# Kernel optimization log

Measured on AMD Instinct MI355X. Metric: run time of the kernel, lower is better.

Reference implementation:

```python
import jax, jax.numpy as jnp
import numpy as np

NUM_GROUPS = 8
EPS = 1e-5


def group_norm(x, gamma, beta):
    # x: [B, C, H, W]
    B, C, H, W = x.shape
    xg = x.reshape(B, NUM_GROUPS, C // NUM_GROUPS, H, W)
    mean = xg.mean(axis=(2, 3, 4), keepdims=True)
    var = xg.var(axis=(2, 3, 4), keepdims=True)
    xn = (xg - mean) * jax.lax.rsqrt(var + EPS)
    xn = xn.reshape(B, C, H, W)
    return xn * gamma[None, :, None, None] + beta[None, :, None, None]


def setup_inputs() -> dict:
    key = jax.random.key(0)
    ks = jax.random.split(key, 7)
    B, C, H, W = 4, 512, 64, 64
    x = jax.random.normal(ks[0], (B, C, H, W), dtype=jnp.float32)
    gamma = jnp.ones((C,), dtype=jnp.float32)
    beta = jnp.zeros((C,), dtype=jnp.float32)
    w_qkv = jax.random.normal(ks[1], (3 * C, C), dtype=jnp.float32) * (1.0 / np.sqrt(C))
    b_qkv = jax.random.normal(ks[2], (3 * C,), dtype=jnp.float32) * 0.01
    w_proj = jax.random.normal(ks[3], (C, C), dtype=jnp.float32) * (1.0 / np.sqrt(C))
    b_proj = jax.random.normal(ks[4], (C,), dtype=jnp.float32) * 0.01
    return {"x": x, "gamma": gamma, "beta": beta, "w_qkv": w_qkv,
            "b_qkv": b_qkv, "w_proj": w_proj, "b_proj": b_proj}


def reference(x, gamma, beta, w_qkv, b_qkv, w_proj, b_proj):
    B, C, H, W = x.shape
    N = H * W
    h = group_norm(x, gamma, beta)                       # [B,C,H,W]
    hf = h.reshape(B, C, N)                              # [B,C,N]
    # 1x1 conv == channel-wise linear map
    qkv = jnp.einsum('oc,bcn->bon', w_qkv, hf) + b_qkv[None, :, None]  # [B,3C,N]
    q, k, v = jnp.split(qkv, 3, axis=1)                  # each [B,C,N]
    q = q.transpose(0, 2, 1)                             # [B,N,C]
    v = v.transpose(0, 2, 1)                             # [B,N,C]
    scale = C ** (-0.5)
    attn = jax.nn.softmax(jnp.einsum('bnc,bcm->bnm', q, k) * scale, axis=-1)  # [B,N,N]
    out = jnp.einsum('bnm,bmc->bnc', attn, v)            # [B,N,C]
    out = out.transpose(0, 2, 1).reshape(B, C, H, W)
    proj = jnp.einsum('oc,bchw->bohw', w_proj, out) + b_proj[None, :, None, None]
    return x + proj
```

## Files before the change

kernel.cpp:

```cpp
#include <hip/hip_runtime.h>

typedef __attribute__((ext_vector_type(8))) short bf16x8;
typedef __attribute__((ext_vector_type(4))) float f32x4;
typedef __attribute__((ext_vector_type(4))) short s16x4;
using u16 = unsigned short;
using u8 = unsigned char;

#define DEVINL static __device__ __forceinline__

DEVINL u16 f2bf(float f) {
  union { float f; unsigned u; } v; v.f = f;
  unsigned r = v.u + 0x7FFFu + ((v.u >> 16) & 1u);
  return (u16)(r >> 16);
}

DEVINL u8 f2e4m3_sw(float f) {
  union { float f; unsigned u; } v; v.f = f;
  unsigned s = (v.u >> 24) & 0x80u;
  float a = fabsf(f);
  a = fminf(a, 448.f);
  union { float f; unsigned u; } b; b.f = a;
  unsigned bu = b.u + 0x7FFFFu + ((b.u >> 20) & 1u);
  unsigned e = bu >> 23;
  unsigned r;
  if (e >= 121) {
    r = ((e - 120) << 3) | ((bu >> 20) & 7u);
    if (r > 0x7Eu) r = 0x7Eu;
  } else {
    r = (unsigned)(a * 512.f + 0.5f);
    if (r > 7u) r = 8u;
  }
  return (u8)(r | s);
}

#if __has_builtin(__builtin_amdgcn_cvt_pk_fp8_f32)
DEVINL u8 f2e4m3(float f) {
  int p = __builtin_amdgcn_cvt_pk_fp8_f32(f, f, 0, false);
  return (u8)(p & 0xFF);
}
#else
DEVINL u8 f2e4m3(float f) { return f2e4m3_sw(f); }
#endif

DEVINL float bf2f(u16 h) {
  union { unsigned u; float f; } v; v.u = ((unsigned)h) << 16; return v.f;
}

DEVINL void gload16(const u16* g, u16* l) {
  __builtin_amdgcn_global_load_lds((const __attribute__((address_space(1))) void*)g,
                                   (__attribute__((address_space(3))) void*)l,
                                   16, 0, 0);
}
DEVINL void gload16b(const u8* g, u8* l) {
  __builtin_amdgcn_global_load_lds((const __attribute__((address_space(1))) void*)g,
                                   (__attribute__((address_space(3))) void*)l,
                                   16, 0, 0);
}

__global__ __launch_bounds__(256) void gn_stats1_k(const float* __restrict__ x,
                                                   float* __restrict__ psum,
                                                   float* __restrict__ psumsq) {
  const int blk = blockIdx.x;
  const float4* p4 = (const float4*)(x + (size_t)(blk >> 4) * (64 * 4096))
                     + (size_t)(blk & 15) * 4096;
  float s = 0.f, ss = 0.f;
  #pragma unroll
  for (int i = 0; i < 16; ++i) {
    float4 v = p4[i*256 + threadIdx.x];
    s  += v.x + v.y + v.z + v.w;
    ss += v.x*v.x + v.y*v.y + v.z*v.z + v.w*v.w;
  }
  #pragma unroll
  for (int off = 32; off > 0; off >>= 1) {
    s  += __shfl_down(s, off, 64);
    ss += __shfl_down(ss, off, 64);
  }
  __shared__ float rs[4], rss[4];
  const int lane = threadIdx.x & 63, w = threadIdx.x >> 6;
  if (lane == 0) { rs[w] = s; rss[w] = ss; }
  __syncthreads();
  if (threadIdx.x == 0) {
    psum[blk]   = rs[0]+rs[1]+rs[2]+rs[3];
    psumsq[blk] = rss[0]+rss[1]+rss[2]+rss[3];
  }
}

__global__ void gn_stats2_k(const float* __restrict__ psum,
                            const float* __restrict__ psumsq,
                            float* __restrict__ stats) {
  const int bg = threadIdx.x;
  if (bg >= 32) return;
  float s = 0.f, ss = 0.f;
  #pragma unroll
  for (int p = 0; p < 16; ++p) { s += psum[bg*16+p]; ss += psumsq[bg*16+p]; }
  const float inv = 1.f / 262144.f;
  float mean = s * inv;
  float var  = ss * inv - mean * mean;
  stats[bg*2]   = mean;
  stats[bg*2+1] = rsqrtf(var + 1e-5f);
}

__global__ __launch_bounds__(256) void gn_apply_k(const float* __restrict__ x,
                                                  const float* __restrict__ gamma,
                                                  const float* __restrict__ beta,
                                                  const float* __restrict__ stats,
                                                  u16* __restrict__ hT,
                                                  u8* __restrict__ hT8, int useF8) {
  __shared__ u16 tile[64][68];
  const int b = blockIdx.z, ct = blockIdx.y, nt = blockIdx.x;
  const int t = threadIdx.x;
  const float mean = stats[(b*8 + ct)*2 + 0];
  const float rstd = stats[(b*8 + ct)*2 + 1];
  const float* xb = x + ((size_t)b*512 + (size_t)ct*64) * 4096 + nt*64;
  #pragma unroll
  for (int i = 0; i < 4; ++i) {
    int idx = i*256 + t;
    int cl = idx >> 4, nl4 = idx & 15;
    float4 v = *(const float4*)(xb + (size_t)cl*4096 + nl4*4);
    float g = gamma[ct*64 + cl], bb = beta[ct*64 + cl];
    s16x4 o;
    o.x = (short)f2bf((v.x - mean) * rstd * g + bb);
    o.y = (short)f2bf((v.y - mean) * rstd * g + bb);
    o.z = (short)f2bf((v.z - mean) * rstd * g + bb);
    o.w = (short)f2bf((v.w - mean) * rstd * g + bb);
    *(s16x4*)(&tile[cl][nl4*4]) = o;
  }
  __syncthreads();
  if (useF8) {
    u8* o = hT8 + ((size_t)b*4096 + (size_t)nt*64) * 512 + ct*64;
    #pragma unroll
    for (int i = 0; i < 16; ++i) {
      int idx = i*256 + t; int nl = idx >> 6, cl = idx & 63;
      o[(size_t)nl*512 + cl] = f2e4m3(bf2f(tile[cl][nl]));
    }
  } else {
    u16* o = hT + ((size_t)b*4096 + (size_t)nt*64) * 512 + ct*64;
    #pragma unroll
    for (int i = 0; i < 16; ++i) {
      int idx = i*256 + t; int nl = idx >> 6, cl = idx & 63;
      o[(size_t)nl*512 + cl] = tile[cl][nl];
    }
  }
}

__global__ __launch_bounds__(256) void cast_w_k(const float* __restrict__ wq,
                                                const float* __restrict__ wp,
                                                u16* __restrict__ wqb,
                                                u16* __restrict__ wpb,
                                                u8* __restrict__ wq8,
                                                u8* __restrict__ wp8, int useF8) {
  int i = blockIdx.x*256 + threadIdx.x;
  if (useF8) {
    if (i < 1536*512) wq8[i] = f2e4m3(wq[i]);
    if (i < 512*512)  wp8[i] = f2e4m3(wp[i]);
  } else {
    if (i < 1536*512) wqb[i] = f2bf(wq[i]);
    if (i < 512*512)  wpb[i] = f2bf(wp[i]);
  }
}

DEVINL void gemm_nt_core(const u16* __restrict__ A, int lda,
                         const u16* __restrict__ B, int ldb,
                         int K, u16* As, u16* Bs, f32x4 acc[4][4]) {
  const int tid = threadIdx.x;
  const int lane = tid & 63, w = tid >> 6;
  const int wr = w >> 1, wc = w & 1;
  const int fr = lane & 15, fk = lane >> 4;
  for (int kt = 0; kt < K; kt += 64) {
    #pragma unroll
    for (int i = 0; i < 4; ++i) {
      int ch = i*256 + tid;
      int row = ch >> 3, kc = ch & 7;
      gload16(A + (size_t)row*lda + kt + kc*8, As + ch*8);
      gload16(B + (size_t)row*ldb + kt + kc*8, Bs + ch*8);
    }
    __syncthreads();
    #pragma unroll
    for (int kk = 0; kk < 2; ++kk) {
      bf16x8 af[4], bfg[4];
      #pragma unroll
      for (int i = 0; i < 4; ++i)
        af[i] = *(const bf16x8*)(As + ((wr*64 + i*16 + fr)*64 + kk*32 + fk*8));
      #pragma unroll
      for (int j = 0; j < 4; ++j)
        bfg[j] = *(const bf16x8*)(Bs + ((wc*64 + j*16 + fr)*64 + kk*32 + fk*8));
      #pragma unroll
      for (int i = 0; i < 4; ++i)
        #pragma unroll
        for (int j = 0; j < 4; ++j)
          acc[i][j] = __builtin_amdgcn_mfma_f32_16x16x32_bf16(af[i], bfg[j], acc[i][j], 0, 0, 0);
    }
    __syncthreads();
  }
}

#define GEMM_PROLOGUE() \
  __shared__ __align__(16) u16 As[128*64]; \
  __shared__ __align__(16) u16 Bs[128*64]; \
  f32x4 acc[4][4] = {}; \
  const int tid = threadIdx.x; \
  const int lane = tid & 63, w = tid >> 6; \
  const int wr = w >> 1, wc = w & 1; \
  const int fr = lane & 15, fk = lane >> 4; \
  (void)lane;

#define MFMA8(a, b, c) __builtin_amdgcn_mfma_f32_16x16x32_fp8_fp8((a), (b), (c), 0, 0, 0)

DEVINL void gemm_nt_f8(const u8* __restrict__ A, int lda,
                       const u8* __restrict__ B, int ldb,
                       int K, u8* Af, u8* Bf, f32x4 acc[4][4]) {
  const int tid = threadIdx.x;
  const int lane = tid & 63, w = tid >> 6;
  const int wr = w >> 1, wc = w & 1;
  const int fr = lane & 15, fk = lane >> 4;
  for (int kt = 0; kt < K; kt += 128) {
    #pragma unroll
    for (int q = 0; q < 4; ++q) {
      int c = q*256 + tid;
      int row = c >> 3, s16 = c & 7;
      int kc = s16 ^ ((row >> 1) & 7);
      gload16b(A + (size_t)row*lda + kt + kc*16, Af + c*16);
      gload16b(B + (size_t)row*ldb + kt + kc*16, Bf + c*16);
    }
    __syncthreads();
    #pragma unroll
    for (int kk = 0; kk < 4; ++kk) {
      long long a8[4], b8[4];
      #pragma unroll
      for (int i = 0; i < 4; ++i) {
        int row = wr*64 + i*16 + fr;
        int s16r = (kk*2 + (fk>>1)) ^ ((row>>1)&7);
        a8[i] = *(const long long*)(Af + row*128 + (s16r<<4) + ((fk&1)<<3));
      }
      #pragma unroll
      for (int j = 0; j < 4; ++j) {
        int row = wc*64 + j*16 + fr;
        int s16r = (kk*2 + (fk>>1)) ^ ((row>>1)&7);
        b8[j] = *(const long long*)(Bf + row*128 + (s16r<<4) + ((fk&1)<<3));
      }
      #pragma unroll
      for (int i = 0; i < 4; ++i)
        #pragma unroll
        for (int j = 0; j < 4; ++j)
          acc[i][j] = MFMA8(a8[i], b8[j], acc[i][j]);
    }
    __syncthreads();
  }
}

__global__ __launch_bounds__(256) void k_qkv(const u16* __restrict__ hT,
                                             const u16* __restrict__ wq,
                                             const float* __restrict__ bqkv,
                                             u16* __restrict__ qT, u16* __restrict__ kT,
                                             u16* __restrict__ vb) {
  GEMM_PROLOGUE();
  const int bz = blockIdx.z;
  const int rowBase = blockIdx.y * 128, colBase = blockIdx.x * 128;
  gemm_nt_core(hT + ((size_t)bz*4096 + rowBase)*512, 512,
               wq + (size_t)colBase*512, 512, 512, As, Bs, acc);
  #pragma unroll
  for (int i = 0; i < 4; ++i)
    #pragma unroll
    for (int j = 0; j < 4; ++j)
      #pragma unroll
      for (int r = 0; r < 4; ++r) {
        int n = rowBase + wr*64 + i*16 + fk*4 + r;
        int o = colBase + wc*64 + j*16 + fr;
        u16 u = f2bf(acc[i][j][r] + bqkv[o]);
        if (o < 512)       qT[((size_t)bz*4096 + n)*512 + o]          = u;
        else if (o < 1024) kT[((size_t)bz*4096 + n)*512 + (o - 512)]  = u;
        else               vb[((size_t)bz*512 + (o - 1024))*4096 + n] = u;
      }
}

__global__ __launch_bounds__(256) void k_qkv_f8(const u8* __restrict__ hT8,
                                                const u8* __restrict__ wq8,
                                                const float* __restrict__ bqkv,
                                                u8* __restrict__ qF8, u8* __restrict__ kF8,
                                                u8* __restrict__ vF8) {
  __shared__ __align__(16) u8 Af[128*128];
  __shared__ __align__(16) u8 Bf[128*128];
  f32x4 acc[4][4] = {};
  const int tid = threadIdx.x;
  const int lane = tid & 63, w = tid >> 6;
  const int wr = w >> 1, wc = w & 1;
  const int fr = lane & 15, fk = lane >> 4;
  const int bz = blockIdx.z;
  const int rowBase = blockIdx.y * 128, colBase = blockIdx.x * 128;
  gemm_nt_f8(hT8 + ((size_t)bz*4096 + rowBase)*512, 512,
             wq8 + (size_t)colBase*512, 512, 512, Af, Bf, acc);
  #pragma unroll
  for (int i = 0; i < 4; ++i)
    #pragma unroll
    for (int j = 0; j < 4; ++j)
      #pragma unroll
      for (int r = 0; r < 4; ++r) {
        int n = rowBase + wr*64 + i*16 + fk*4 + r;
        int o = colBase + wc*64 + j*16 + fr;
        u8 u = f2e4m3(acc[i][j][r] + bqkv[o]);
        if (o < 512)       qF8[((size_t)bz*4096 + n)*512 + o]          = u;
        else if (o < 1024) kF8[((size_t)bz*4096 + n)*512 + (o - 512)]  = u;
        else               vF8[((size_t)bz*512 + (o - 1024))*4096 + n] = u;
      }
}

__global__ __launch_bounds__(512) void k_scores_f8(const u8* __restrict__ qF8,
                                                   const u8* __restrict__ kF8,
                                                   u8* __restrict__ E8) {
  __shared__ __align__(16) u8 Af[128*64];
  __shared__ __align__(16) u8 Bf[128*64];
  f32x4 acc[2][4] = {};
  const int tid = threadIdx.x;
  const int lane = tid & 63, w = tid >> 6;
  const int wr = w >> 1, wc = w & 1;
  const int fr = lane & 15, fk = lane >> 4;
  const int bz = blockIdx.z;
  int f = blockIdx.y * 32 + blockIdx.x;
  int L = (f & 7) * 128 + (f >> 3);
  const int rowBase = (L >> 5) * 128, colBase = (L & 31) * 128;
  const u8* qa = qF8 + (size_t)bz*4096*512 + (size_t)rowBase*512;
  const u8* ka = kF8 + (size_t)bz*4096*512 + (size_t)colBase*512;
  u8* Eb = E8 + (size_t)bz*4096*4096;

  for (int kt = 0; kt < 512; kt += 64) {
    {
      int c = tid;
      int row = c >> 2, s16 = c & 3;
      int kc = s16 ^ ((row >> 1) & 3);
      gload16b(qa + (size_t)row*512 + kt + kc*16, Af + c*16);
      gload16b(ka + (size_t)row*512 + kt + kc*16, Bf + c*16);
    }
    __syncthreads();
    #pragma unroll
    for (int kk = 0; kk < 2; ++kk) {
      long long a8[2], b8[4];
      #pragma unroll
      for (int i = 0; i < 2; ++i) {
        int row = wr*32 + i*16 + fr;
        a8[i] = *(const long long*)(Af + row*64 +
                ((((kk*2 + (fk>>1)) ^ ((row>>1)&3)) << 4) | ((fk&1) << 3)));
      }
      #pragma unroll
      for (int j = 0; j < 4; ++j) {
        int row = wc*64 + j*16 + fr;
        b8[j] = *(const long long*)(Bf + row*64 +
                ((((kk*2 + (fk>>1)) ^ ((row>>1)&3)) << 4) | ((fk&1) << 3)));
      }
      #pragma unroll
      for (int i = 0; i < 2; ++i)
        #pragma unroll
        for (int j = 0; j < 4; ++j)
          acc[i][j] = MFMA8(a8[i], b8[j], acc[i][j]);
    }
    __syncthreads();
  }

  const float scale = 0.04419417382415922f;
  #pragma unroll
  for (int i = 0; i < 2; ++i)
    #pragma unroll
    for (int r = 0; r < 4; ++r) {
      int nl = rowBase + wr*32 + i*16 + fk*4 + r;
      #pragma unroll
      for (int j = 0; j < 4; ++j) {
        int m = colBase + wc*64 + j*16 + fr;
        Eb[(size_t)nl*4096 + m] = f2e4m3(__expf(acc[i][j][r] * scale));
      }
    }
}

__global__ __launch_bounds__(512) void k_pv_f8(const u8* __restrict__ E8,
                                               const u8* __restrict__ vF8,
                                               u8* __restrict__ attn8) {
  __shared__ __align__(16) u8 Af[128*128];
  __shared__ __align__(16) u8 Bf[128*128];
  f32x4 acc[2][4] = {};
  f32x4 acs[2] = {};
  const long long ONES = 0x3838383838383838LL;
  const int tid = threadIdx.x;
  const int lane = tid & 63, w = tid >> 6;
  const int wr = w >> 1, wc = w & 1;
  const int fr = lane & 15, fk = lane >> 4;
  const int bz = blockIdx.z;
  int f = blockIdx.y * 4 + blockIdx.x;
  int L = (f & 7) * 16 + (f >> 3);
  const int rowBase = (L >> 2) * 128, colBase = (L & 3) * 128;
  const u8* Eb = E8 + (size_t)bz*4096*4096 + (size_t)rowBase*4096;
  const u8* vbb = vF8 + (size_t)bz*512*4096 + (size_t)colBase*4096;
  u8* ab = attn8 + (size_t)bz*4096*512;

  for (int kt = 0; kt < 4096; kt += 128) {
    #pragma unroll
    for (int q = 0; q < 2; ++q) {
      int c = q*512 + tid;
      int row = c >> 3, s16 = c & 7;
      int kc = s16 ^ ((row >> 1) & 7);
      gload16b(Eb + (size_t)row*4096 + kt + kc*16, Af + c*16);
      gload16b(vbb + (size_t)row*4096 + kt + kc*16, Bf + c*16);
    }
    __syncthreads();
    #pragma unroll
    for (int kk = 0; kk < 4; ++kk) {
      long long a8[2], b8[4];
      #pragma unroll
      for (int i = 0; i < 2; ++i) {
        int row = wr*32 + i*16 + fr;
        int s16r = (kk*2 + (fk>>1)) ^ ((row>>1)&7);
        a8[i] = *(const long long*)(Af + row*128 + (s16r<<4) + ((fk&1)<<3));
      }
      #pragma unroll
      for (int j = 0; j < 4; ++j) {
        int row = wc*64 + j*16 + fr;
        int s16r = (kk*2 + (fk>>1)) ^ ((row>>1)&7);
        b8[j] = *(const long long*)(Bf + row*128 + (s16r<<4) + ((fk&1)<<3));
      }
      #pragma unroll
      for (int i = 0; i < 2; ++i) {
        #pragma unroll
        for (int j = 0; j < 4; ++j)
          acc[i][j] = MFMA8(a8[i], b8[j], acc[i][j]);
        acs[i] = MFMA8(a8[i], ONES, acs[i]);
      }
    }
    __syncthreads();
  }

  #pragma unroll
  for (int i = 0; i < 2; ++i)
    #pragma unroll
    for (int r = 0; r < 4; ++r) {
      int nl = rowBase + wr*32 + i*16 + fk*4 + r;
      float rinv = 1.0f / acs[i][r];
      #pragma unroll
      for (int j = 0; j < 4; ++j) {
        int d = colBase + wc*64 + j*16 + fr;
        ab[(size_t)nl*512 + d] = f2e4m3(acc[i][j][r] * rinv);
      }
    }
}

__global__ __launch_bounds__(256) void k_proj_f8(const u8* __restrict__ wp8,
                                                 const u8* __restrict__ attn8,
                                                 const float* __restrict__ bproj,
                                                 const float* __restrict__ x,
                                                 float* __restrict__ out) {
  __shared__ __align__(16) u8 Af[128*128];
  __shared__ __align__(16) u8 Bf[128*128];
  f32x4 acc[4][4] = {};
  const int tid = threadIdx.x;
  const int lane = tid & 63, w = tid >> 6;
  const int wr = w >> 1, wc = w & 1;
  const int fr = lane & 15, fk = lane >> 4;
  const int bz = blockIdx.z;
  const int rowBase = blockIdx.y * 128, colBase = blockIdx.x * 128;
  gemm_nt_f8(wp8 + (size_t)rowBase*512, 512,
             attn8 + ((size_t)bz*4096 + colBase)*512, 512, 512, Af, Bf, acc);
  #pragma unroll
  for (int i = 0; i < 4; ++i)
    #pragma unroll
    for (int j = 0; j < 4; ++j)
      #pragma unroll
      for (int r = 0; r < 4; ++r) {
        int o = rowBase + wr*64 + i*16 + fk*4 + r;
        int n = colBase + wc*64 + j*16 + fr;
        size_t idx = ((size_t)bz*512 + o)*4096 + n;
        out[idx] = acc[i][j][r] + bproj[o] + x[idx];
      }
}

__global__ __launch_bounds__(256) void k_scores(const u16* __restrict__ qT,
                                                const u16* __restrict__ kT,
                                                u16* __restrict__ E,
                                                float* __restrict__ lsum,
                                                long long qkStride, long long eStride,
                                                int lsStride) {
  GEMM_PROLOGUE();
  const int bz = blockIdx.z;
  const u16* q0 = qT + (size_t)bz * qkStride;
  const u16* k0 = kT + (size_t)bz * qkStride;
  u16* Eb = E + (size_t)bz * eStride;
  float* ls = lsum + (size_t)bz * lsStride;
  const int rowBase = blockIdx.y * 128, colBase = blockIdx.x * 128;
  gemm_nt_core(q0 + (size_t)rowBase*512, 512, k0 + (size_t)colBase*512, 512,
               512, As, Bs, acc);
  const float scale = 0.04419417382415922f;
  #pragma unroll
  for (int i = 0; i < 4; ++i)
    #pragma unroll
    for (int r = 0; r < 4; ++r) {
      int nl = rowBase + wr*64 + i*16 + fk*4 + r;
      float s = 0.f;
      #pragma unroll
      for (int j = 0; j < 4; ++j) {
        int m = colBase + wc*64 + j*16 + fr;
        float e = __expf(acc[i][j][r] * scale);
        Eb[(size_t)nl*4096 + m] = f2bf(e);
        s += e;
      }
      s += __shfl_xor(s, 1, 64);
      s += __shfl_xor(s, 2, 64);
      s += __shfl_xor(s, 4, 64);
      s += __shfl_xor(s, 8, 64);
      if (fr == 0) atomicAdd(&ls[nl], s);
    }
}

__global__ __launch_bounds__(256) void k_pv(const u16* __restrict__ E,
                                            const u16* __restrict__ vb,
                                            const float* __restrict__ lsum,
                                            u16* __restrict__ attnb,
                                            long long eStride, long long vStride,
                                            int lsStride, long long aStride) {
  GEMM_PROLOGUE();
  const int bz = blockIdx.z;
  const u16* Eb = E + (size_t)bz * eStride;
  const u16* vbb = vb + (size_t)bz * vStride;
  const float* ls = lsum + (size_t)bz * lsStride;
  u16* ab = attnb + (size_t)bz * aStride;
  const int rowBase = blockIdx.y * 128, colBase = blockIdx.x * 128;
  gemm_nt_core(Eb + (size_t)rowBase*4096, 4096, vbb + (size_t)colBase*4096, 4096,
               4096, As, Bs, acc);
  #pragma unroll
  for (int i = 0; i < 4; ++i)
    #pragma unroll
    for (int r = 0; r < 4; ++r) {
      int nl = rowBase + wr*64 + i*16 + fk*4 + r;
      float rinv = 1.0f / ls[nl];
      #pragma unroll
      for (int j = 0; j < 4; ++j) {
        int d = colBase + wc*64 + j*16 + fr;
        ab[(size_t)nl*512 + d] = f2bf(acc[i][j][r] * rinv);
      }
    }
}

__global__ __launch_bounds__(256) void k_proj(const u16* __restrict__ wp,
                                              const u16* __restrict__ attn,
                                              const float* __restrict__ bproj,
                                              const float* __restrict__ x,
                                              float* __restrict__ out) {
  GEMM_PROLOGUE();
  const int bz = blockIdx.z;
  const int rowBase = blockIdx.y * 128, colBase = blockIdx.x * 128;
  gemm_nt_core(wp + (size_t)rowBase*512, 512,
               attn + ((size_t)bz*4096 + colBase)*512, 512, 512, As, Bs, acc);
  #pragma unroll
  for (int i = 0; i < 4; ++i)
    #pragma unroll
    for (int j = 0; j < 4; ++j)
      #pragma unroll
      for (int r = 0; r < 4; ++r) {
        int o = rowBase + wr*64 + i*16 + fk*4 + r;
        int n = colBase + wc*64 + j*16 + fr;
        size_t idx = ((size_t)bz*512 + o)*4096 + n;
        out[idx] = acc[i][j][r] + bproj[o] + x[idx];
      }
}

extern "C" void kernel_launch(void* const* d_in, const int* in_sizes, int n_in,
                              void* d_out, int out_size, void* d_ws, size_t ws_size,
                              hipStream_t stream) {
  const float* x      = (const float*)d_in[0];
  const float* gamma  = (const float*)d_in[1];
  const float* beta   = (const float*)d_in[2];
  const float* w_qkv  = (const float*)d_in[3];
  const float* b_qkv  = (const float*)d_in[4];
  const float* w_proj = (const float*)d_in[5];
  const float* b_proj = (const float*)d_in[6];
  float* out = (float*)d_out;
  char* ws = (char*)d_ws;

  size_t off = 0;
  u16* wqb   = (u16*)(ws + off); off += (size_t)1536*512*2;
  u16* wpb   = (u16*)(ws + off); off += (size_t)512*512*2;
  u8*  wq8   = (u8*)(ws + off);  off += (size_t)1536*512;
  u8*  wp8   = (u8*)(ws + off);  off += (size_t)512*512;
  float* stats = (float*)(ws + off); off += 256;
  float* psum  = (float*)(ws + off); off += 512*4;
  float* psumsq= (float*)(ws + off); off += 512*4;
  float* lsum  = (float*)(ws + off); off += (size_t)4*4096*4;
  u16* hT    = (u16*)(ws + off);
  u16* attn  = hT;
  off += (size_t)4*4096*512*2;
  u16* qT    = (u16*)(ws + off); off += (size_t)4*4096*512*2;
  u16* kT    = (u16*)(ws + off); off += (size_t)4*4096*512*2;
  u16* vb    = (u16*)(ws + off); off += (size_t)4*4096*512*2;
  u16* E     = (u16*)(ws + off);
  size_t avail = ws_size > off ? ws_size - off : 0;
  const int useF8 = (avail >= (size_t)4*4096*4096) ? 1 : 0;
  u8* hT8  = (u8*)hT;
  u8* attn8 = hT8;
  u8* qF8 = (u8*)qT;
  u8* kF8 = (u8*)kT;
  u8* vF8 = (u8*)vb;
  u8* E8  = (u8*)E;

  gn_stats1_k<<<512, 256, 0, stream>>>(x, psum, psumsq);
  gn_stats2_k<<<1, 32, 0, stream>>>(psum, psumsq, stats);
  gn_apply_k<<<dim3(64, 8, 4), 256, 0, stream>>>(x, gamma, beta, stats, hT, hT8, useF8);
  cast_w_k<<<3072, 256, 0, stream>>>(w_qkv, w_proj, wqb, wpb, wq8, wp8, useF8);

  if (useF8) {
    k_qkv_f8<<<dim3(12, 32, 4), 256, 0, stream>>>(hT8, wq8, b_qkv, qF8, kF8, vF8);
    k_scores_f8<<<dim3(32, 32, 4), 512, 0, stream>>>(qF8, kF8, E8);
    k_pv_f8<<<dim3(4, 32, 4), 512, 0, stream>>>(E8, vF8, attn8);
    k_proj_f8<<<dim3(32, 4, 4), 256, 0, stream>>>(wp8, attn8, b_proj, x, out);
  } else {
    k_qkv<<<dim3(12, 32, 4), 256, 0, stream>>>(hT, wqb, b_qkv, qT, kT, vb);
    int CH = 4096;
    while (CH > 128 && (size_t)CH*4096*2 > avail) CH >>= 1;
    for (int b = 0; b < 4; ++b) {
      for (int c0 = 0; c0 < 4096; c0 += CH) {
        (void)hipMemsetAsync(lsum, 0, (size_t)CH * sizeof(float), stream);
        k_scores<<<dim3(32, CH/128, 1), 256, 0, stream>>>(
            qT + ((size_t)b*4096 + c0)*512, kT + (size_t)b*4096*512, E, lsum, 0, 0, 0);
        k_pv<<<dim3(4, CH/128, 1), 256, 0, stream>>>(
            E, vb + (size_t)b*512*4096, lsum, attn + ((size_t)b*4096 + c0)*512, 0, 0, 0, 0);
      }
    }
    k_proj<<<dim3(32, 4, 4), 256, 0, stream>>>(wpb, attn, b_proj, x, out);
  }
}
```

Baseline: 214.7 us.

## Double-buffer LDS tiles in FP8 scores and PV GEMM kernels

Both FP8 attention GEMM kernels now hold two LDS buffers for the A and B tiles. Each iteration prefetches the next K-slice into the alternate buffer while computing MFMAs on the current one. The goal is to hide global-to-LDS load latency behind compute and drop one barrier per iteration. In exchange, LDS footprint doubles (64KB per block in the PV kernel), which may limit occupancy.

```diff
diff --git a/kernel.cpp b/kernel.cpp
--- a/kernel.cpp
+++ b/kernel.cpp
@@ -307,8 +307,8 @@
 __global__ __launch_bounds__(512) void k_scores_f8(const u8* __restrict__ qF8,
                                                    const u8* __restrict__ kF8,
                                                    u8* __restrict__ E8) {
-  __shared__ __align__(16) u8 Af[128*64];
-  __shared__ __align__(16) u8 Bf[128*64];
+  __shared__ __align__(16) u8 Af[2][128*64];
+  __shared__ __align__(16) u8 Bf[2][128*64];
   f32x4 acc[2][4] = {};
   const int tid = threadIdx.x;
   const int lane = tid & 63, w = tid >> 6;
@@ -322,28 +322,36 @@
   const u8* ka = kF8 + (size_t)bz*4096*512 + (size_t)colBase*512;
   u8* Eb = E8 + (size_t)bz*4096*4096;
 
-  for (int kt = 0; kt < 512; kt += 64) {
-    {
-      int c = tid;
-      int row = c >> 2, s16 = c & 3;
-      int kc = s16 ^ ((row >> 1) & 3);
-      gload16b(qa + (size_t)row*512 + kt + kc*16, Af + c*16);
-      gload16b(ka + (size_t)row*512 + kt + kc*16, Bf + c*16);
-    }
-    __syncthreads();
+  const int srow = tid >> 2, ss16 = tid & 3;
+  const int skc = ss16 ^ ((srow >> 1) & 3);
+
+  gload16b(qa + (size_t)srow*512 + 0 + skc*16, Af[0] + tid*16);
+  gload16b(ka + (size_t)srow*512 + 0 + skc*16, Bf[0] + tid*16);
+  __syncthreads();
+
+  #pragma unroll 1
+  for (int t = 0; t < 8; ++t) {
+    const int cur = t & 1;
+    if (t < 7) {
+      int ktn = (t + 1) * 64;
+      gload16b(qa + (size_t)srow*512 + ktn + skc*16, Af[cur ^ 1] + tid*16);
+      gload16b(ka + (size_t)srow*512 + ktn + skc*16, Bf[cur ^ 1] + tid*16);
+    }
+    const u8* Ap = Af[cur];
+    const u8* Bp = Bf[cur];
     #pragma unroll
     for (int kk = 0; kk < 2; ++kk) {
       long long a8[2], b8[4];
       #pragma unroll
       for (int i = 0; i < 2; ++i) {
         int row = wr*32 + i*16 + fr;
-        a8[i] = *(const long long*)(Af + row*64 +
+        a8[i] = *(const long long*)(Ap + row*64 +
                 ((((kk*2 + (fk>>1)) ^ ((row>>1)&3)) << 4) | ((fk&1) << 3)));
       }
       #pragma unroll
       for (int j = 0; j < 4; ++j) {
         int row = wc*64 + j*16 + fr;
-        b8[j] = *(const long long*)(Bf + row*64 +
+        b8[j] = *(const long long*)(Bp + row*64 +
                 ((((kk*2 + (fk>>1)) ^ ((row>>1)&3)) << 4) | ((fk&1) << 3)));
       }
       #pragma unroll
@@ -372,8 +380,8 @@
 __global__ __launch_bounds__(512) void k_pv_f8(const u8* __restrict__ E8,
                                                const u8* __restrict__ vF8,
                                                u8* __restrict__ attn8) {
-  __shared__ __align__(16) u8 Af[128*128];
-  __shared__ __align__(16) u8 Bf[128*128];
+  __shared__ __align__(16) u8 Af[2][128*128];
+  __shared__ __align__(16) u8 Bf[2][128*128];
   f32x4 acc[2][4] = {};
   f32x4 acs[2] = {};
   const long long ONES = 0x3838383838383838LL;
@@ -389,16 +397,28 @@
   const u8* vbb = vF8 + (size_t)bz*512*4096 + (size_t)colBase*4096;
   u8* ab = attn8 + (size_t)bz*4096*512;
 
-  for (int kt = 0; kt < 4096; kt += 128) {
-    #pragma unroll
-    for (int q = 0; q < 2; ++q) {
-      int c = q*512 + tid;
-      int row = c >> 3, s16 = c & 7;
-      int kc = s16 ^ ((row >> 1) & 7);
-      gload16b(Eb + (size_t)row*4096 + kt + kc*16, Af + c*16);
-      gload16b(vbb + (size_t)row*4096 + kt + kc*16, Bf + c*16);
-    }
-    __syncthreads();
+  const int c0 = tid, c1 = 512 + tid;
+  const int r0 = c0 >> 3, k0 = (c0 & 7) ^ ((r0 >> 1) & 7);
+  const int r1 = c1 >> 3, k1 = (c1 & 7) ^ ((r1 >> 1) & 7);
+
+  gload16b(Eb + (size_t)r0*4096 + 0 + k0*16, Af[0] + c0*16);
+  gload16b(vbb + (size_t)r0*4096 + 0 + k0*16, Bf[0] + c0*16);
+  gload16b(Eb + (size_t)r1*4096 + 0 + k1*16, Af[0] + c1*16);
+  gload16b(vbb + (size_t)r1*4096 + 0 + k1*16, Bf[0] + c1*16);
+  __syncthreads();
+
+  #pragma unroll 1
+  for (int t = 0; t < 32; ++t) {
+    const int cur = t & 1;
+    if (t < 31) {
+      int ktn = (t + 1) * 128;
+      gload16b(Eb + (size_t)r0*4096 + ktn + k0*16, Af[cur ^ 1] + c0*16);
+      gload16b(vbb + (size_t)r0*4096 + ktn + k0*16, Bf[cur ^ 1] + c0*16);
+      gload16b(Eb + (size_t)r1*4096 + ktn + k1*16, Af[cur ^ 1] + c1*16);
+      gload16b(vbb + (size_t)r1*4096 + ktn + k1*16, Bf[cur ^ 1] + c1*16);
+    }
+    const u8* Ap = Af[cur];
+    const u8* Bp = Bf[cur];
     #pragma unroll
     for (int kk = 0; kk < 4; ++kk) {
       long long a8[2], b8[4];
@@ -406,13 +426,13 @@
       for (int i = 0; i < 2; ++i) {
         int row = wr*32 + i*16 + fr;
         int s16r = (kk*2 + (fk>>1)) ^ ((row>>1)&7);
-        a8[i] = *(const long long*)(Af + row*128 + (s16r<<4) + ((fk&1)<<3));
+        a8[i] = *(const long long*)(Ap + row*128 + (s16r<<4) + ((fk&1)<<3));
       }
       #pragma unroll
       for (int j = 0; j < 4; ++j) {
         int row = wc*64 + j*16 + fr;
         int s16r = (kk*2 + (fk>>1)) ^ ((row>>1)&7);
-        b8[j] = *(const long long*)(Bf + row*128 + (s16r<<4) + ((fk&1)<<3));
+        b8[j] = *(const long long*)(Bp + row*128 + (s16r<<4) + ((fk&1)<<3));
       }
       #pragma unroll
       for (int i = 0; i < 2; ++i) {
```

After: 215.0 us. No clear change (+0.1%).
